# Performance work log

Measured on AMD Instinct MI355X. Metric: run time of the kernel, lower is better.

Reference implementation:

```python
import jax, jax.numpy as jnp
import numpy as np

T, B, D, H, L = 512, 64, 1024, 512, 5  # H = hidden_size // 2


def setup_inputs() -> dict:
    key = jax.random.key(0)
    ks = jax.random.split(key, 9)
    sD = 1.0 / np.sqrt(D)
    sH = 1.0 / np.sqrt(H)
    u = lambda k, shape, s: jax.random.uniform(k, shape, jnp.float32, -s, s)
    return {
        "x": jax.random.normal(ks[0], (T, B, D), jnp.float32),
        # first-layer input projections (only layer 0 has W_H / W_C)
        "W_H_w": u(ks[1], (D, H), sD),
        "W_H_b": u(ks[2], (H,), sD),
        "W_C_w": u(ks[3], (D, H), sD),
        "W_C_b": u(ks[4], (H,), sD),
        # recurrent projections for all L layers, stacked
        "R_H_w": u(ks[5], (L, H, H), sH),
        "R_H_b": u(ks[6], (L, H), sH),
        "R_C_w": u(ks[7], (L, H, H), sH),
        "R_C_b": u(ks[8], (L, H), sH),
    }


def reference(x, W_H_w, W_H_b, W_C_w, W_C_b, R_H_w, R_H_b, R_C_w, R_C_b):
    # x: [T, B, D]; one RHN time step applies L highway micro-layers.
    def cell_stack(x_t, hidden):
        # layer 0: uses input projections + recurrent projections
        hl = jnp.tanh(x_t @ W_H_w + W_H_b + hidden @ R_H_w[0] + R_H_b[0])
        tl = jax.nn.sigmoid(x_t @ W_C_w + W_C_b + hidden @ R_C_w[0] + R_C_b[0])
        hidden = hl * tl + hidden * (1.0 - tl)
        # layers 1..L-1: recurrent-only highway layers (small fixed unroll)
        for l in range(1, L):
            hl = jnp.tanh(hidden @ R_H_w[l] + R_H_b[l])
            tl = jax.nn.sigmoid(hidden @ R_C_w[l] + R_C_b[l])
            hidden = hl * tl + hidden * (1.0 - tl)
        return hidden

    def step(h, x_t):
        h = cell_stack(x_t, h)
        return h, h

    h0 = jnp.zeros((x.shape[1], H), x.dtype)
    # first pass ("lefts"); second pass ("rights") continues from final hidden
    h_mid, lefts = jax.lax.scan(step, h0, x)    # lefts:  [T, B, H]
    _, rights = jax.lax.scan(step, h_mid, x)    # rights: [T, B, H]
    outputs = jnp.concatenate([lefts, rights], axis=2)  # [T, B, 2H]
    hiddens = outputs[-1][None]                          # [1, B, 2H]
    return outputs, hiddens
```

## Files before the change

kernel.cpp:

```cpp
#include <hip/hip_runtime.h>
#include <math.h>

#define T_STEPS 512
#define NL      5

typedef short bf16x8 __attribute__((ext_vector_type(8)));
typedef float f32x4  __attribute__((ext_vector_type(4)));

#define OFF_P     0ull
#define OFF_W     134217728ull
#define OFF_R     (OFF_W + 6291456ull)
#define OFF_WBC   (OFF_R + 15728640ull)
#define OFF_RBC   (OFF_WBC + 4096ull)
#define OFF_H     (OFF_RBC + 20480ull)
#define OFF_FLAGS (OFF_H + 393216ull)

#define WPLANE 1048576
#define RPLANE 2621440
#define HBUFSTRIDE 98304
#define RGSLICE 24576

__device__ __forceinline__ unsigned bf_rne(float f) {
    unsigned u = __float_as_uint(f);
    unsigned r = u + 0x7FFFu + ((u >> 16) & 1u);
    return r >> 16;
}
__device__ __forceinline__ float bf_to_f(unsigned bits) {
    return __uint_as_float(bits << 16);
}
__device__ __forceinline__ void split3(float f, short& s0, short& s1, short& s2) {
    unsigned b0 = bf_rne(f);
    float r1 = f - bf_to_f(b0);
    unsigned b1 = bf_rne(r1);
    float r2 = r1 - bf_to_f(b1);
    unsigned b2 = bf_rne(r2);
    s0 = (short)b0; s1 = (short)b1; s2 = (short)b2;
}
__device__ __forceinline__ float fast_sigmoid(float x) { return 1.0f / (1.0f + __expf(-x)); }
__device__ __forceinline__ float fast_tanh(float x)    { return 2.0f / (1.0f + __expf(-2.0f * x)) - 1.0f; }

__global__ void rhn_prep(const float* __restrict__ WHw, const float* __restrict__ WHb,
                         const float* __restrict__ WCw, const float* __restrict__ WCb,
                         const float* __restrict__ RHw, const float* __restrict__ RHb,
                         const float* __restrict__ RCw, const float* __restrict__ RCb,
                         short* __restrict__ Wt, short* __restrict__ Rt,
                         float* __restrict__ wbc, float* __restrict__ rbc,
                         short* __restrict__ hbuf, unsigned* __restrict__ flags)
{
    long long idx = (long long)blockIdx.x * blockDim.x + threadIdx.x;
    if (idx < WPLANE) {
        int n = (int)(idx >> 10), d = (int)(idx & 1023);
        float v = (n < 512) ? WHw[d * 512 + n] : WCw[d * 512 + (n - 512)];
        short s0, s1, s2; split3(v, s0, s1, s2);
        Wt[idx] = s0; Wt[WPLANE + idx] = s1; Wt[2 * WPLANE + idx] = s2;
        return;
    }
    idx -= WPLANE;
    if (idx < RPLANE) {
        int l = (int)(idx >> 19);
        int rem = (int)(idx & 524287);
        int cc = rem >> 9, k = rem & 511;
        float v = (cc < 512) ? RHw[(l * 512 + k) * 512 + cc]
                             : RCw[(l * 512 + k) * 512 + (cc - 512)];
        short s0, s1, s2; split3(v, s0, s1, s2);
        Rt[idx] = s0; Rt[RPLANE + idx] = s1; Rt[2 * RPLANE + idx] = s2;
        return;
    }
    idx -= RPLANE;
    if (idx < 1024) { wbc[idx] = (idx < 512) ? WHb[idx] : WCb[idx - 512]; return; }
    idx -= 1024;
    if (idx < 5120) {
        int l = (int)(idx >> 10), c = (int)(idx & 1023);
        rbc[idx] = (c < 512) ? RHb[l * 512 + c] : RCb[l * 512 + (c - 512)];
        return;
    }
    idx -= 5120;
    if (idx < 2 * HBUFSTRIDE) { hbuf[idx] = 0; return; }
    idx -= 2 * HBUFSTRIDE;
    if (idx < 1024) { flags[idx] = 0u; return; }
}

__global__ void __launch_bounds__(256) rhn_proj(const float* __restrict__ x,
                                                const short* __restrict__ Wt,
                                                const float* __restrict__ wbc,
                                                float* __restrict__ P)
{
    const int bx = blockIdx.x;
    const int by = blockIdx.y;
    const int tid = threadIdx.x, wave = tid >> 6, lane = tid & 63;
    const int n = lane & 15, quad = lane >> 4;
    const int rowA = by * 64 + wave * 16 + n;
    const float* xrow = x + (long long)rowA * 1024;

    f32x4 acc[4];
#pragma unroll
    for (int nt = 0; nt < 4; ++nt) {
        float b = wbc[bx * 64 + nt * 16 + n];
        acc[nt][0] = b; acc[nt][1] = b; acc[nt][2] = b; acc[nt][3] = b;
    }

    for (int ks = 0; ks < 32; ++ks) {
        const int ko = ks * 32 + quad * 8;
        f32x4 f0 = *(const f32x4*)(xrow + ko);
        f32x4 f1 = *(const f32x4*)(xrow + ko + 4);
        bf16x8 a0, a1, a2;
#pragma unroll
        for (int i = 0; i < 4; ++i) {
            short u0, u1, u2;
            split3(f0[i], u0, u1, u2);
            a0[i] = u0; a1[i] = u1; a2[i] = u2;
            split3(f1[i], u0, u1, u2);
            a0[4 + i] = u0; a1[4 + i] = u1; a2[4 + i] = u2;
        }
#pragma unroll
        for (int nt = 0; nt < 4; ++nt) {
            const long long wi = (long long)(bx * 64 + nt * 16 + n) * 1024 + ko;
            bf16x8 b0 = *(const bf16x8*)(Wt + wi);
            bf16x8 b1 = *(const bf16x8*)(Wt + WPLANE + wi);
            bf16x8 b2 = *(const bf16x8*)(Wt + 2 * WPLANE + wi);
            acc[nt] = __builtin_amdgcn_mfma_f32_16x16x32_bf16(a2, b0, acc[nt], 0, 0, 0);
            acc[nt] = __builtin_amdgcn_mfma_f32_16x16x32_bf16(a1, b1, acc[nt], 0, 0, 0);
            acc[nt] = __builtin_amdgcn_mfma_f32_16x16x32_bf16(a0, b2, acc[nt], 0, 0, 0);
            acc[nt] = __builtin_amdgcn_mfma_f32_16x16x32_bf16(a1, b0, acc[nt], 0, 0, 0);
            acc[nt] = __builtin_amdgcn_mfma_f32_16x16x32_bf16(a0, b1, acc[nt], 0, 0, 0);
            acc[nt] = __builtin_amdgcn_mfma_f32_16x16x32_bf16(a0, b0, acc[nt], 0, 0, 0);
        }
    }
#pragma unroll
    for (int nt = 0; nt < 4; ++nt)
#pragma unroll
        for (int r = 0; r < 4; ++r)
            P[(long long)(by * 64 + wave * 16 + quad * 4 + r) * 1024 + bx * 64 + nt * 16 + n] = acc[nt][r];
}

__global__ void __launch_bounds__(256, 1) rhn_rec(const float* __restrict__ P,
                                                  const short* __restrict__ Rt,
                                                  const float* __restrict__ rbc,
                                                  short* __restrict__ hbuf,
                                                  unsigned* __restrict__ flags,
                                                  float* __restrict__ out)
{
    __shared__ short hsm[24960];
    const int wg = blockIdx.x;
    const int rg = wg >> 4;
    const int cg = wg & 15;
    const int tid = threadIdx.x;
    const int wave = tid >> 6;
    const int lane = tid & 63;
    const int n = lane & 15;
    const int quad = lane >> 4;
    const bool isH = (n < 8);
    const int jH = cg * 32 + wave * 8 + (n & 7);
    const int ccol = isH ? jH : (512 + jH);
    const int rowloc = quad * 4;
    const int grow = rg * 16 + rowloc;
    const int aoff = n * 520 + quad * 8;

    float hold[4] = {0.f, 0.f, 0.f, 0.f};
    float* hidOut = out + 33554432;
    unsigned* const myflag = flags + (wg << 4);
    const unsigned* const gflags = flags + (rg << 8);

    unsigned stage = 0;
#pragma unroll 1
    for (int step = 0; step < 2 * T_STEPS; ++step) {
        const int pass = (step >= T_STEPS) ? 1 : 0;
        const int t = step - pass * T_STEPS;
        const float* Pt = P + (long long)t * (64 * 1024);
#pragma unroll 1
        for (int l = 0; l < NL; ++l) {
            {
                const unsigned long long* hsrc = (const unsigned long long*)
                    (hbuf + (stage & 1u) * HBUFSTRIDE + rg * RGSLICE);
                unsigned long long v[24];
#pragma unroll
                for (int it = 0; it < 24; ++it)
                    v[it] = __hip_atomic_load(hsrc + (it * 256 + tid),
                                              __ATOMIC_RELAXED, __HIP_MEMORY_SCOPE_AGENT);
#pragma unroll
                for (int it = 0; it < 24; ++it) {
                    const int c = it * 256 + tid;
                    const int p = c >> 11, r = (c >> 7) & 15, k4 = c & 127;
                    *(unsigned long long*)&hsm[(p * 16 + r) * 520 + k4 * 4] = v[it];
                }
            }
            __syncthreads();

            f32x4 acc0, acc1, acc2;
            {
                float b0 = rbc[l * 1024 + ccol];
                acc0[0] = b0; acc0[1] = b0; acc0[2] = b0; acc0[3] = b0;
                acc1[0] = 0.f; acc1[1] = 0.f; acc1[2] = 0.f; acc1[3] = 0.f;
                acc2[0] = 0.f; acc2[1] = 0.f; acc2[2] = 0.f; acc2[3] = 0.f;
            }
            if (l == 0) {
#pragma unroll
                for (int r = 0; r < 4; ++r)
                    acc0[r] += Pt[(grow + r) * 1024 + ccol];
            }
            const short* bp = Rt + ((l * 1024 + ccol) << 9) + quad * 8;
#pragma unroll
            for (int ks = 0; ks < 16; ++ks) {
                const int o = ks * 32;
                bf16x8 a0 = *(const bf16x8*)&hsm[aoff + o];
                bf16x8 a1 = *(const bf16x8*)&hsm[8320 + aoff + o];
                bf16x8 a2 = *(const bf16x8*)&hsm[16640 + aoff + o];
                bf16x8 b0 = *(const bf16x8*)(bp + o);
                bf16x8 b1 = *(const bf16x8*)(bp + RPLANE + o);
                bf16x8 b2 = *(const bf16x8*)(bp + 2 * RPLANE + o);
                acc0 = __builtin_amdgcn_mfma_f32_16x16x32_bf16(a0, b0, acc0, 0, 0, 0);
                acc1 = __builtin_amdgcn_mfma_f32_16x16x32_bf16(a1, b0, acc1, 0, 0, 0);
                acc2 = __builtin_amdgcn_mfma_f32_16x16x32_bf16(a2, b0, acc2, 0, 0, 0);
                acc0 = __builtin_amdgcn_mfma_f32_16x16x32_bf16(a0, b1, acc0, 0, 0, 0);
                acc1 = __builtin_amdgcn_mfma_f32_16x16x32_bf16(a1, b1, acc1, 0, 0, 0);
                acc2 = __builtin_amdgcn_mfma_f32_16x16x32_bf16(a0, b2, acc2, 0, 0, 0);
            }

            float hn[4];
#pragma unroll
            for (int r = 0; r < 4; ++r) {
                float p = (acc2[r] + acc1[r]) + acc0[r];
                float a = isH ? fast_tanh(p) : fast_sigmoid(p);
                float o = __shfl_xor(a, 8, 64);
                hn[r] = a * o + hold[r] * (1.0f - o);
            }
            if (isH) {
                unsigned pk[3][4];
#pragma unroll
                for (int r = 0; r < 4; ++r) {
                    hold[r] = hn[r];
                    short s0, s1, s2; split3(hn[r], s0, s1, s2);
                    pk[0][r] = (unsigned short)s0;
                    pk[1][r] = (unsigned short)s1;
                    pk[2][r] = (unsigned short)s2;
                }
#pragma unroll
                for (int p2 = 0; p2 < 3; ++p2)
#pragma unroll
                    for (int r = 0; r < 4; ++r) {
                        unsigned nb = __shfl_xor(pk[p2][r], 1, 64);
                        pk[p2][r] |= (nb << 16);
                    }
                if (!(n & 1)) {
                    unsigned* hwU = (unsigned*)hbuf + ((stage & 1u) ^ 1u) * 49152
                                    + rg * 12288 + (jH >> 1);
#pragma unroll
                    for (int p2 = 0; p2 < 3; ++p2)
#pragma unroll
                        for (int r = 0; r < 4; ++r)
                            __hip_atomic_store(hwU + p2 * 4096 + (rowloc + r) * 256,
                                               pk[p2][r], __ATOMIC_RELAXED,
                                               __HIP_MEMORY_SCOPE_AGENT);
                }
                if (l == NL - 1) {
#pragma unroll
                    for (int r = 0; r < 4; ++r) {
                        out[(long long)(t * 64 + grow + r) * 1024 + pass * 512 + jH] = hn[r];
                        if (t == T_STEPS - 1)
                            hidOut[(grow + r) * 1024 + pass * 512 + jH] = hn[r];
                    }
                }
            }

            ++stage;
            __syncthreads();
            if (tid == 0)
                __hip_atomic_store(myflag, stage, __ATOMIC_RELAXED, __HIP_MEMORY_SCOPE_AGENT);
            bool done = false;
            while (!done) {
                unsigned vv = stage;
                if (lane < 16)
                    vv = __hip_atomic_load(gflags + lane * 16,
                                           __ATOMIC_RELAXED, __HIP_MEMORY_SCOPE_AGENT);
                done = (__ballot(vv >= stage) == ~0ull);
                if (!done) __builtin_amdgcn_s_sleep(1);
            }
        }
    }
}

extern "C" void kernel_launch(void* const* d_in, const int* in_sizes, int n_in,
                              void* d_out, int out_size, void* d_ws, size_t ws_size,
                              hipStream_t stream)
{
    const float* x   = (const float*)d_in[0];
    const float* WHw = (const float*)d_in[1];
    const float* WHb = (const float*)d_in[2];
    const float* WCw = (const float*)d_in[3];
    const float* WCb = (const float*)d_in[4];
    const float* RHw = (const float*)d_in[5];
    const float* RHb = (const float*)d_in[6];
    const float* RCw = (const float*)d_in[7];
    const float* RCb = (const float*)d_in[8];

    char* ws = (char*)d_ws;
    float*    Pbuf  = (float*)(ws + OFF_P);
    short*    Wt    = (short*)(ws + OFF_W);
    short*    Rt    = (short*)(ws + OFF_R);
    float*    wbc   = (float*)(ws + OFF_WBC);
    float*    rbc   = (float*)(ws + OFF_RBC);
    short*    hbuf  = (short*)(ws + OFF_H);
    unsigned* flags = (unsigned*)(ws + OFF_FLAGS);
    float*    outp  = (float*)d_out;

    rhn_prep<<<15132, 256, 0, stream>>>(WHw, WHb, WCw, WCb, RHw, RHb, RCw, RCb,
                                        Wt, Rt, wbc, rbc, hbuf, flags);
    rhn_proj<<<dim3(16, 512), 256, 0, stream>>>(x, Wt, wbc, Pbuf);

    void* args[] = {&Pbuf, &Rt, &rbc, &hbuf, &flags, &outp};
    hipLaunchCooperativeKernel(reinterpret_cast<void*>(rhn_rec), dim3(64), dim3(256),
                               args, 0, stream);
}
```

Before: 43.98 ms.

## Keep recurrent weights in registers and split K across waves over 256 blocks

The recurrent kernel now launches 256 workgroups instead of 64. Each workgroup covers 8 hidden columns, and its four waves each take a quarter of the K dimension. All five layers' bf16-split weight slices are held in registers for the whole run. The old LDS staging of the full hidden state is gone: each wave loads its A fragments straight from global memory, and partial sums are reduced through LDS into wave 0. Next-step projection values are prefetched, flag stores use release and the wait ends with an acquire fence. The goal is to remove the per-layer weight reloads and global-to-LDS copies on the serial critical path, at the cost of more workgroups in the grid barrier, a cross-wave reduction, heavy register use, and launching without the cooperative guarantee.

```diff
diff --git a/kernel.cpp b/kernel.cpp
--- a/kernel.cpp
+++ b/kernel.cpp
@@ -6,6 +6,7 @@
 
 typedef short bf16x8 __attribute__((ext_vector_type(8)));
 typedef float f32x4  __attribute__((ext_vector_type(4)));
+typedef unsigned long long u64;
 
 #define OFF_P     0ull
 #define OFF_W     134217728ull
@@ -38,6 +39,12 @@
 }
 __device__ __forceinline__ float fast_sigmoid(float x) { return 1.0f / (1.0f + __expf(-x)); }
 __device__ __forceinline__ float fast_tanh(float x)    { return 2.0f / (1.0f + __expf(-2.0f * x)) - 1.0f; }
+__device__ __forceinline__ bf16x8 asbf(u64 lo, u64 hi) {
+    u64 q[2] = {lo, hi};
+    bf16x8 r;
+    __builtin_memcpy(&r, q, 16);
+    return r;
+}
 
 __global__ void rhn_prep(const float* __restrict__ WHw, const float* __restrict__ WHb,
                          const float* __restrict__ WCw, const float* __restrict__ WCb,
@@ -140,88 +147,111 @@
                                                   unsigned* __restrict__ flags,
                                                   float* __restrict__ out)
 {
-    __shared__ short hsm[24960];
-    const int wg = blockIdx.x;
-    const int rg = wg >> 4;
-    const int cg = wg & 15;
-    const int tid = threadIdx.x;
-    const int wave = tid >> 6;
+    __shared__ float2 red[18][64];
+    const int wg   = blockIdx.x;
+    const int rg   = wg >> 6;
+    const int cg   = wg & 63;
+    const int tid  = threadIdx.x;
+    const int wv   = tid >> 6;
     const int lane = tid & 63;
-    const int n = lane & 15;
+    const int n    = lane & 15;
     const int quad = lane >> 4;
     const bool isH = (n < 8);
-    const int jH = cg * 32 + wave * 8 + (n & 7);
+    const int jH   = cg * 8 + (n & 7);
     const int ccol = isH ? jH : (512 + jH);
     const int rowloc = quad * 4;
     const int grow = rg * 16 + rowloc;
-    const int aoff = n * 520 + quad * 8;
+
+    bf16x8 w[NL][3][4];
+#pragma unroll
+    for (int l = 0; l < NL; ++l) {
+        const short* bp = Rt + ((l * 1024 + ccol) << 9) + wv * 128 + quad * 8;
+#pragma unroll
+        for (int p = 0; p < 3; ++p)
+#pragma unroll
+            for (int ks = 0; ks < 4; ++ks)
+                w[l][p][ks] = *(const bf16x8*)(bp + p * RPLANE + ks * 32);
+    }
+    float rb[NL];
+#pragma unroll
+    for (int l = 0; l < NL; ++l) rb[l] = rbc[l * 1024 + ccol];
 
     float hold[4] = {0.f, 0.f, 0.f, 0.f};
+    float hn[4];
+    float pv[4];
+#pragma unroll
+    for (int r = 0; r < 4; ++r) pv[r] = P[(grow + r) * 1024 + ccol];
+
     float* hidOut = out + 33554432;
-    unsigned* const myflag = flags + (wg << 4);
+    unsigned* const myflag = flags + (wg << 2);
     const unsigned* const gflags = flags + (rg << 8);
+    const u64* const hb = (const u64*)hbuf;
+    const int abase = rg * (RGSLICE / 4) + n * 128 + wv * 32 + quad * 2;
 
     unsigned stage = 0;
-#pragma unroll 1
-    for (int step = 0; step < 2 * T_STEPS; ++step) {
-        const int pass = (step >= T_STEPS) ? 1 : 0;
-        const int t = step - pass * T_STEPS;
-        const float* Pt = P + (long long)t * (64 * 1024);
-#pragma unroll 1
-        for (int l = 0; l < NL; ++l) {
-            {
-                const unsigned long long* hsrc = (const unsigned long long*)
-                    (hbuf + (stage & 1u) * HBUFSTRIDE + rg * RGSLICE);
-                unsigned long long v[24];
-#pragma unroll
-                for (int it = 0; it < 24; ++it)
-                    v[it] = __hip_atomic_load(hsrc + (it * 256 + tid),
-                                              __ATOMIC_RELAXED, __HIP_MEMORY_SCOPE_AGENT);
-#pragma unroll
-                for (int it = 0; it < 24; ++it) {
-                    const int c = it * 256 + tid;
-                    const int p = c >> 11, r = (c >> 7) & 15, k4 = c & 127;
-                    *(unsigned long long*)&hsm[(p * 16 + r) * 520 + k4 * 4] = v[it];
-                }
-            }
-            __syncthreads();
-
-            f32x4 acc0, acc1, acc2;
-            {
-                float b0 = rbc[l * 1024 + ccol];
-                acc0[0] = b0; acc0[1] = b0; acc0[2] = b0; acc0[3] = b0;
-                acc1[0] = 0.f; acc1[1] = 0.f; acc1[2] = 0.f; acc1[3] = 0.f;
-                acc2[0] = 0.f; acc2[1] = 0.f; acc2[2] = 0.f; acc2[3] = 0.f;
-            }
-            if (l == 0) {
-#pragma unroll
-                for (int r = 0; r < 4; ++r)
-                    acc0[r] += Pt[(grow + r) * 1024 + ccol];
-            }
-            const short* bp = Rt + ((l * 1024 + ccol) << 9) + quad * 8;
-#pragma unroll
-            for (int ks = 0; ks < 16; ++ks) {
-                const int o = ks * 32;
-                bf16x8 a0 = *(const bf16x8*)&hsm[aoff + o];
-                bf16x8 a1 = *(const bf16x8*)&hsm[8320 + aoff + o];
-                bf16x8 a2 = *(const bf16x8*)&hsm[16640 + aoff + o];
-                bf16x8 b0 = *(const bf16x8*)(bp + o);
-                bf16x8 b1 = *(const bf16x8*)(bp + RPLANE + o);
-                bf16x8 b2 = *(const bf16x8*)(bp + 2 * RPLANE + o);
-                acc0 = __builtin_amdgcn_mfma_f32_16x16x32_bf16(a0, b0, acc0, 0, 0, 0);
-                acc1 = __builtin_amdgcn_mfma_f32_16x16x32_bf16(a1, b0, acc1, 0, 0, 0);
-                acc2 = __builtin_amdgcn_mfma_f32_16x16x32_bf16(a2, b0, acc2, 0, 0, 0);
-                acc0 = __builtin_amdgcn_mfma_f32_16x16x32_bf16(a0, b1, acc0, 0, 0, 0);
-                acc1 = __builtin_amdgcn_mfma_f32_16x16x32_bf16(a1, b1, acc1, 0, 0, 0);
-                acc2 = __builtin_amdgcn_mfma_f32_16x16x32_bf16(a0, b2, acc2, 0, 0, 0);
-            }
-
-            float hn[4];
+
+    auto layer = [&](const bf16x8 (&wl)[3][4], const float rbl,
+                     const int lfirst, const int llast,
+                     const int t, const int pass, const int step) {
+        const u64* src = hb + (stage & 1u) * (HBUFSTRIDE / 4) + abase;
+        u64 va[3][4][2];
+#pragma unroll
+        for (int p = 0; p < 3; ++p)
+#pragma unroll
+            for (int ks = 0; ks < 4; ++ks)
+#pragma unroll
+                for (int h2 = 0; h2 < 2; ++h2)
+                    va[p][ks][h2] = __hip_atomic_load(src + p * 2048 + ks * 8 + h2,
+                                                      __ATOMIC_RELAXED,
+                                                      __HIP_MEMORY_SCOPE_AGENT);
+
+        f32x4 acc[3];
+#pragma unroll
+        for (int r = 0; r < 4; ++r) {
+            float s = 0.f;
+            if (wv == 0) { s = rbl; if (lfirst) s += pv[r]; }
+            acc[0][r] = s; acc[1][r] = 0.f; acc[2][r] = 0.f;
+        }
+#pragma unroll
+        for (int ks = 0; ks < 4; ++ks) {
+            bf16x8 a0 = asbf(va[0][ks][0], va[0][ks][1]);
+            bf16x8 a1 = asbf(va[1][ks][0], va[1][ks][1]);
+            bf16x8 a2 = asbf(va[2][ks][0], va[2][ks][1]);
+            acc[0] = __builtin_amdgcn_mfma_f32_16x16x32_bf16(a0, wl[0][ks], acc[0], 0, 0, 0);
+            acc[1] = __builtin_amdgcn_mfma_f32_16x16x32_bf16(a1, wl[0][ks], acc[1], 0, 0, 0);
+            acc[2] = __builtin_amdgcn_mfma_f32_16x16x32_bf16(a2, wl[0][ks], acc[2], 0, 0, 0);
+            acc[0] = __builtin_amdgcn_mfma_f32_16x16x32_bf16(a0, wl[1][ks], acc[0], 0, 0, 0);
+            acc[1] = __builtin_amdgcn_mfma_f32_16x16x32_bf16(a1, wl[1][ks], acc[1], 0, 0, 0);
+            acc[2] = __builtin_amdgcn_mfma_f32_16x16x32_bf16(a0, wl[2][ks], acc[2], 0, 0, 0);
+        }
+
+        if (wv != 0) {
+            const int rbase = (wv - 1) * 6;
+#pragma unroll
+            for (int p = 0; p < 3; ++p)
+#pragma unroll
+                for (int rp = 0; rp < 2; ++rp)
+                    red[rbase + p * 2 + rp][lane] =
+                        make_float2(acc[p][rp * 2], acc[p][rp * 2 + 1]);
+        }
+        __syncthreads();
+
+        if (wv == 0) {
+#pragma unroll
+            for (int w2 = 0; w2 < 3; ++w2)
+#pragma unroll
+                for (int p = 0; p < 3; ++p)
+#pragma unroll
+                    for (int rp = 0; rp < 2; ++rp) {
+                        float2 v2 = red[w2 * 6 + p * 2 + rp][lane];
+                        acc[p][rp * 2]     += v2.x;
+                        acc[p][rp * 2 + 1] += v2.y;
+                    }
 #pragma unroll
             for (int r = 0; r < 4; ++r) {
-                float p = (acc2[r] + acc1[r]) + acc0[r];
-                float a = isH ? fast_tanh(p) : fast_sigmoid(p);
-                float o = __shfl_xor(a, 8, 64);
+                float pf = (acc[2][r] + acc[1][r]) + acc[0][r];
+                float a  = isH ? fast_tanh(pf) : fast_sigmoid(pf);
+                float o  = __shfl_xor(a, 8, 64);
                 hn[r] = a * o + hold[r] * (1.0f - o);
             }
             if (isH) {
@@ -252,30 +282,52 @@
                                                pk[p2][r], __ATOMIC_RELAXED,
                                                __HIP_MEMORY_SCOPE_AGENT);
                 }
-                if (l == NL - 1) {
-#pragma unroll
-                    for (int r = 0; r < 4; ++r) {
-                        out[(long long)(t * 64 + grow + r) * 1024 + pass * 512 + jH] = hn[r];
-                        if (t == T_STEPS - 1)
-                            hidOut[(grow + r) * 1024 + pass * 512 + jH] = hn[r];
-                    }
-                }
             }
-
-            ++stage;
-            __syncthreads();
-            if (tid == 0)
-                __hip_atomic_store(myflag, stage, __ATOMIC_RELAXED, __HIP_MEMORY_SCOPE_AGENT);
+        }
+
+        ++stage;
+        __syncthreads();
+        if (tid == 0)
+            __hip_atomic_store(myflag, stage, __ATOMIC_RELEASE, __HIP_MEMORY_SCOPE_AGENT);
+
+        if (llast && wv == 0 && isH) {
+#pragma unroll
+            for (int r = 0; r < 4; ++r) {
+                out[(long long)(t * 64 + grow + r) * 1024 + pass * 512 + jH] = hn[r];
+                if (t == T_STEPS - 1)
+                    hidOut[(grow + r) * 1024 + pass * 512 + jH] = hn[r];
+            }
+        }
+        if (llast && wv == 0 && step < 2 * T_STEPS - 1) {
+            const int sn = step + 1;
+            const int tn = (sn >= T_STEPS) ? (sn - T_STEPS) : sn;
+            const float* Ptn = P + (long long)tn * 65536;
+#pragma unroll
+            for (int r = 0; r < 4; ++r) pv[r] = Ptn[(grow + r) * 1024 + ccol];
+        }
+
+        {
             bool done = false;
             while (!done) {
-                unsigned vv = stage;
-                if (lane < 16)
-                    vv = __hip_atomic_load(gflags + lane * 16,
-                                           __ATOMIC_RELAXED, __HIP_MEMORY_SCOPE_AGENT);
+                unsigned vv = __hip_atomic_load(gflags + (lane << 2),
+                                                __ATOMIC_RELAXED, __HIP_MEMORY_SCOPE_AGENT);
                 done = (__ballot(vv >= stage) == ~0ull);
                 if (!done) __builtin_amdgcn_s_sleep(1);
             }
         }
+        __builtin_amdgcn_fence(__ATOMIC_ACQUIRE, "agent");
+        __builtin_amdgcn_sched_barrier(0);
+    };
+
+#pragma unroll 1
+    for (int step = 0; step < 2 * T_STEPS; ++step) {
+        const int pass = (step >= T_STEPS) ? 1 : 0;
+        const int t = step - pass * T_STEPS;
+        layer(w[0], rb[0], 1, 0, t, pass, step);
+        layer(w[1], rb[1], 0, 0, t, pass, step);
+        layer(w[2], rb[2], 0, 0, t, pass, step);
+        layer(w[3], rb[3], 0, 0, t, pass, step);
+        layer(w[4], rb[4], 0, 1, t, pass, step);
     }
 }
 
@@ -307,7 +359,5 @@
                                         Wt, Rt, wbc, rbc, hbuf, flags);
     rhn_proj<<<dim3(16, 512), 256, 0, stream>>>(x, Wt, wbc, Pbuf);
 
-    void* args[] = {&Pbuf, &Rt, &rbc, &hbuf, &flags, &outp};
-    hipLaunchCooperativeKernel(reinterpret_cast<void*>(rhn_rec), dim3(64), dim3(256),
-                               args, 0, stream);
-}
+    rhn_rec<<<dim3(256), dim3(256), 0, stream>>>(Pbuf, Rt, rbc, hbuf, flags, outp);
+}
```

After: 75.25 ms. +71.1%, slower.
